# Performance work log

Measured on AMD Instinct MI355X. Metric: run time of the kernel, lower is better.

## Reference

```python
import jax, jax.numpy as jnp
import numpy as np
from functools import partial

E = 256   # input_size (embedding dim)
H = 256   # hidden_size
T = 4096  # number of admissions (GRU sequence length, batch=1)


def _gru_seq(x_seq, w_ih, w_hh, b_ih, b_hh):
    """Single-layer unidirectional GRU over x_seq [T, E] with batch=1.
    PyTorch gate order: r, z, n. Returns outputs [T, H]."""
    h_dim = w_hh.shape[1]
    # input projections are step-independent: precompute [T, 3H]
    gi_all = x_seq @ w_ih.T + b_ih

    def step(h, gi):
        gh = h @ w_hh.T + b_hh
        i_r, i_z, i_n = jnp.split(gi, 3)
        h_r, h_z, h_n = jnp.split(gh, 3)
        r = jax.nn.sigmoid(i_r + h_r)
        z = jax.nn.sigmoid(i_z + h_z)
        n = jnp.tanh(i_n + r * h_n)
        h_new = (1.0 - z) * n + z * h
        return h_new, h_new

    h0 = jnp.zeros((h_dim,), x_seq.dtype)
    _, out = jax.lax.scan(step, h0, gi_all)
    return out  # [T, H]


def setup_inputs() -> dict:
    key = jax.random.key(0)
    ks = jax.random.split(key, 16)
    u = lambda k, shape, s: jax.random.uniform(k, shape, jnp.float32, -s, s)
    sg = 1.0 / np.sqrt(H)  # PyTorch GRU/Linear init scale
    inp = {}
    # embeddings initialized uniform(-0.1, 0.1) per initialize_weights()
    inp["emb_diag"] = u(ks[0], (20000, E), 0.1)
    inp["emb_proc"] = u(ks[1], (15000, E), 0.1)  # unused by forward (source bug), kept for fidelity
    # GRU params (layer 0), gate order r,z,n
    inp["wih_d"] = u(ks[2], (3 * H, E), sg)
    inp["whh_d"] = u(ks[3], (3 * H, H), sg)
    inp["bih_d"] = u(ks[4], (3 * H,), sg)
    inp["bhh_d"] = u(ks[5], (3 * H,), sg)
    inp["wih_p"] = u(ks[6], (3 * H, E), sg)
    inp["whh_p"] = u(ks[7], (3 * H, H), sg)
    inp["bih_p"] = u(ks[8], (3 * H,), sg)
    inp["bhh_p"] = u(ks[9], (3 * H,), sg)
    # linear_embedding: ReLU -> Linear(2H, H)
    sl = 1.0 / np.sqrt(2 * H)
    inp["w_lin"] = u(ks[10], (H, 2 * H), sl)
    inp["b_lin"] = u(ks[11], (H,), sl)
    # ragged admission code lists, represented as fixed-length rows
    inp["diag_codes"] = jax.random.randint(ks[12], (T, 32), 0, 20000)
    inp["proc_codes"] = jax.random.randint(ks[13], (T, 16), 0, 15000)
    inp["input_medication"] = jax.random.randint(ks[14], (T, 24), 0, 3000)
    return inp


def reference(emb_diag, emb_proc, wih_d, whh_d, bih_d, bhh_d,
              wih_p, whh_p, bih_p, bhh_p, w_lin, b_lin,
              diag_codes, proc_codes, input_medication):
    # per-admission embedding gather + mean pool (dropout rate 0 -> identity)
    # NOTE: original source uses embedding_diagnoses for BOTH loops (bug kept).
    seq_d = emb_diag[diag_codes].mean(axis=1)  # [T, E]
    seq_p = emb_diag[proc_codes].mean(axis=1)  # [T, E]
    out_d = _gru_seq(seq_d, wih_d, whh_d, bih_d, bhh_d)  # [T, H]
    out_p = _gru_seq(seq_p, wih_p, whh_p, bih_p, bhh_p)  # [T, H]
    patient = jnp.concatenate([out_d, out_p], axis=-1)   # [T, 2H]
    queries = jax.nn.relu(patient) @ w_lin.T + b_lin     # [T, H]
    query = queries[-1:]
    memory_keys = queries[:-1]
    memory_values = input_medication[:-1]
    return (query, memory_keys, memory_values)
```

## Files before the change

kernel.cpp:

```cpp
#include <hip/hip_runtime.h>
#include <hip/hip_fp16.h>

#define T_SEQ 4096
#define E_DIM 256
#define H_DIM 256
#define G3    768

#define KEYS_OFF 256
#define MED_OFF  1048576

#define WS_SEQ_D   0
#define WS_SEQ_P   1048576
#define WS_GI_D    2097152
#define WS_GI_P    5242880
#define WS_PATIENT 8388608

#define SW_SCALE   2016.0f
#define SH_SCALE   127.0f
#define INV_SY     (1.0f / (2016.0f * 127.0f))

__device__ __forceinline__ float fast_rcp(float x) {
#if __has_builtin(__builtin_amdgcn_rcpf)
    return __builtin_amdgcn_rcpf(x);
#else
    return 1.f / x;
#endif
}

__device__ __forceinline__ int sdot4(int a, int b, int c) {
#if __has_builtin(__builtin_amdgcn_sdot4)
    return __builtin_amdgcn_sdot4(a, b, c, false);
#else
    c += ((a << 24) >> 24) * ((b << 24) >> 24);
    c += ((a << 16) >> 24) * ((b << 16) >> 24);
    c += ((a <<  8) >> 24) * ((b <<  8) >> 24);
    c += ( a        >> 24) * ( b        >> 24);
    return c;
#endif
}

__device__ __forceinline__ int pair_sum_i32(int x) {
#if __has_builtin(__builtin_amdgcn_update_dpp)
    x += __builtin_amdgcn_update_dpp(0, x, 0xB1 , 0xF, 0xF, true);
    return x;
#else
    x += __shfl_xor(x, 1);
    return x;
#endif
}

__global__ __launch_bounds__(256) void gather_mean_kernel(
    const float* __restrict__ emb, const int* __restrict__ dcodes,
    const int* __restrict__ pcodes, const int* __restrict__ med,
    float* __restrict__ seq_d, float* __restrict__ seq_p,
    float* __restrict__ med_out)
{
    const int t = blockIdx.x;
    const int e = threadIdx.x;
    __shared__ int cd[32];
    __shared__ int cp[16];
    if (e < 32) cd[e] = dcodes[t * 32 + e];
    else if (e < 48) cp[e - 32] = pcodes[t * 16 + (e - 32)];
    __syncthreads();

    float sd = 0.f;
#pragma unroll 4
    for (int i = 0; i < 32; i++) sd += emb[(size_t)cd[i] * E_DIM + e];
    seq_d[(size_t)t * E_DIM + e] = sd * (1.f / 32.f);

    float sp = 0.f;
#pragma unroll 4
    for (int i = 0; i < 16; i++) sp += emb[(size_t)cp[i] * E_DIM + e];
    seq_p[(size_t)t * E_DIM + e] = sp * (1.f / 16.f);

    if (t < T_SEQ - 1 && e < 24) med_out[t * 24 + e] = (float)med[t * 24 + e];
}

__global__ __launch_bounds__(256) void gemm_gi_kernel(
    const float* __restrict__ seq_d, const float* __restrict__ seq_p,
    const float* __restrict__ wih_d, const float* __restrict__ wih_p,
    const float* __restrict__ bih_d, const float* __restrict__ bih_p,
    const float* __restrict__ bhh_d, const float* __restrict__ bhh_p,
    float* __restrict__ gi_d, float* __restrict__ gi_p)
{
    const int K = E_DIM, N = G3;
    const float* A    = blockIdx.z ? seq_p : seq_d;
    const float* W    = blockIdx.z ? wih_p : wih_d;
    const float* bias = blockIdx.z ? bih_p : bih_d;
    const float* bhh  = blockIdx.z ? bhh_p : bhh_d;
    float*       C    = blockIdx.z ? gi_p  : gi_d;

    __shared__ float As[16][132];
    __shared__ float Bs[16][132];

    const int tid = threadIdx.x;
    const int tx = tid & 15, ty = tid >> 4;
    const int m0 = blockIdx.x * 128, n0 = blockIdx.y * 128;
    const int r = tid >> 2;
    const int c = (tid & 3) << 2;

    float acc[8][8];
#pragma unroll
    for (int i = 0; i < 8; i++)
#pragma unroll
        for (int j = 0; j < 8; j++) acc[i][j] = 0.f;

    for (int k0 = 0; k0 < K; k0 += 16) {
        float4 a0 = *(const float4*)&A[(size_t)(m0 + r) * K + k0 + c];
        float4 a1 = *(const float4*)&A[(size_t)(m0 + r + 64) * K + k0 + c];
        float4 b0 = *(const float4*)&W[(size_t)(n0 + r) * K + k0 + c];
        float4 b1 = *(const float4*)&W[(size_t)(n0 + r + 64) * K + k0 + c];
        As[c + 0][r] = a0.x; As[c + 1][r] = a0.y; As[c + 2][r] = a0.z; As[c + 3][r] = a0.w;
        As[c + 0][r + 64] = a1.x; As[c + 1][r + 64] = a1.y; As[c + 2][r + 64] = a1.z; As[c + 3][r + 64] = a1.w;
        Bs[c + 0][r] = b0.x; Bs[c + 1][r] = b0.y; Bs[c + 2][r] = b0.z; Bs[c + 3][r] = b0.w;
        Bs[c + 0][r + 64] = b1.x; Bs[c + 1][r + 64] = b1.y; Bs[c + 2][r + 64] = b1.z; Bs[c + 3][r + 64] = b1.w;
        __syncthreads();
#pragma unroll
        for (int k = 0; k < 16; k++) {
            float4 aa0 = *(const float4*)&As[k][ty * 8];
            float4 aa1 = *(const float4*)&As[k][ty * 8 + 4];
            float4 bb0 = *(const float4*)&Bs[k][tx * 8];
            float4 bb1 = *(const float4*)&Bs[k][tx * 8 + 4];
            float a[8] = {aa0.x, aa0.y, aa0.z, aa0.w, aa1.x, aa1.y, aa1.z, aa1.w};
            float b[8] = {bb0.x, bb0.y, bb0.z, bb0.w, bb1.x, bb1.y, bb1.z, bb1.w};
#pragma unroll
            for (int i = 0; i < 8; i++)
#pragma unroll
                for (int j = 0; j < 8; j++) acc[i][j] = fmaf(a[i], b[j], acc[i][j]);
        }
        __syncthreads();
    }

#pragma unroll
    for (int i = 0; i < 8; i++) {
        const int m = m0 + ty * 8 + i;
#pragma unroll
        for (int j = 0; j < 8; j++) {
            const int n = n0 + tx * 8 + j;
            const float bb = bias[n] + ((n < 512) ? bhh[n] : 0.f);
            C[(size_t)m * N + n] = acc[i][j] + bb;
        }
    }
}

__global__ __launch_bounds__(256) void quant_whh_kernel(
    const float* __restrict__ whh_d, const float* __restrict__ whh_p,
    unsigned int* __restrict__ w8_d, unsigned int* __restrict__ w8_p)
{
    const int idx = blockIdx.x * 256 + threadIdx.x;
    const float* src = blockIdx.y ? whh_p : whh_d;
    unsigned int* dst = blockIdx.y ? w8_p : w8_d;
    const float4 f = *(const float4*)&src[(size_t)idx * 4];
    const int b0 = (int)rintf(f.x * SW_SCALE) & 0xFF;
    const int b1 = (int)rintf(f.y * SW_SCALE) & 0xFF;
    const int b2 = (int)rintf(f.z * SW_SCALE) & 0xFF;
    const int b3 = (int)rintf(f.w * SW_SCALE) & 0xFF;
    dst[idx] = (unsigned int)(b0 | (b1 << 8) | (b2 << 16) | (b3 << 24));
}

__global__ __launch_bounds__(512, 2) void gru_scan_kernel(
    const unsigned int* __restrict__ w8_d, const unsigned int* __restrict__ w8_p,
    const float* __restrict__ bhh_d, const float* __restrict__ bhh_p,
    const float* __restrict__ gi_d, const float* __restrict__ gi_p,
    float* __restrict__ patient)
{
    const unsigned int* w8 = blockIdx.x ? w8_p : w8_d;
    const float* bhh = blockIdx.x ? bhh_p : bhh_d;
    const float* gi  = blockIdx.x ? gi_p  : gi_d;
    const int col_off = blockIdx.x ? H_DIM : 0;

    const int tid = threadIdx.x;
    const int l   = tid & 63;
    const int w   = tid >> 6;
    const int q   = 32 * w + (l >> 1);
    const int c   = l & 1;

    int wgt[3][32];
#pragma unroll
    for (int g = 0; g < 3; g++) {
        const int4* p = (const int4*)(w8 + ((size_t)(g * 256 + q) * 64 + c * 32));
#pragma unroll
        for (int i = 0; i < 8; i++) {
            const int4 v = p[i];
            wgt[g][4 * i + 0] = v.x;
            wgt[g][4 * i + 1] = v.y;
            wgt[g][4 * i + 2] = v.z;
            wgt[g][4 * i + 3] = v.w;
        }
    }

    __shared__ __align__(16) char hb[2][256];
    if (tid < 256) hb[0][tid] = 0;

    const bool gl = (c == 0);
    float h = 0.f, g0 = 0.f, g1 = 0.f, g2 = 0.f, b2f = 0.f;
    if (gl) {
        b2f = bhh[512 + q];
        g0 = gi[q]; g1 = gi[256 + q]; g2 = gi[512 + q];
    }
    const float* gi_t = gi + G3;
    float*       pat  = patient + col_off;

    const char* hrd = &hb[0][c * 128];

    __syncthreads();

#define GRU_STEP(PAR)                                                           \
    {                                                                           \
        float ng0 = 0.f, ng1 = 0.f, ng2 = 0.f;                                  \
        if (gl) { ng0 = gi_t[q]; ng1 = gi_t[256 + q]; ng2 = gi_t[512 + q]; }    \
        int a0 = 0, a1 = 0, a2 = 0;                                             \
        _Pragma("unroll")                                                       \
        for (int j = 0; j < 8; j++) {                                           \
            const uint4 H = *(const uint4*)(hrd + (PAR) * 256 + j * 16);        \
            const int x0 = (int)H.x, x1 = (int)H.y, x2 = (int)H.z, x3 = (int)H.w; \
            a0 = sdot4(wgt[0][4 * j + 0], x0, a0);                              \
            a0 = sdot4(wgt[0][4 * j + 1], x1, a0);                              \
            a0 = sdot4(wgt[0][4 * j + 2], x2, a0);                              \
            a0 = sdot4(wgt[0][4 * j + 3], x3, a0);                              \
            a1 = sdot4(wgt[1][4 * j + 0], x0, a1);                              \
            a1 = sdot4(wgt[1][4 * j + 1], x1, a1);                              \
            a1 = sdot4(wgt[1][4 * j + 2], x2, a1);                              \
            a1 = sdot4(wgt[1][4 * j + 3], x3, a1);                              \
            a2 = sdot4(wgt[2][4 * j + 0], x0, a2);                              \
            a2 = sdot4(wgt[2][4 * j + 1], x1, a2);                              \
            a2 = sdot4(wgt[2][4 * j + 2], x2, a2);                              \
            a2 = sdot4(wgt[2][4 * j + 3], x3, a2);                              \
        }                                                                       \
        a0 = pair_sum_i32(a0);                                                  \
        a1 = pair_sum_i32(a1);                                                  \
        a2 = pair_sum_i32(a2);                                                  \
        if (gl) {                                                               \
            const float y0 = (float)a0 * INV_SY;                                \
            const float y1 = (float)a1 * INV_SY;                                \
            const float y2 = (float)a2 * INV_SY;                                \
            const float xr = g0 + y0;                 \
            const float xz = g1 + y1;                 \
            const float rr = fast_rcp(1.f + __expf(-xr));                       \
            const float zz = fast_rcp(1.f + __expf(-xz));                       \
            float xn = g2 + rr * (y2 + b2f);                                    \
            xn = fminf(fmaxf(xn, -15.f), 15.f);                                 \
            const float e2 = __expf(2.f * xn);                                  \
            const float nn = (e2 - 1.f) * fast_rcp(e2 + 1.f);                   \
            h = nn + zz * (h - nn);                                             \
            hb[(PAR) ^ 1][q] = (char)(int)rintf(h * SH_SCALE);                  \
            pat[q] = h;                                                         \
            g0 = ng0; g1 = ng1; g2 = ng2;                                       \
        }                                                                       \
        gi_t += G3;                                                             \
        pat += 512;                                                             \
        __syncthreads();                                                        \
    }

    for (int t = 0; t < T_SEQ; t += 2) {
        GRU_STEP(0)
        GRU_STEP(1)
    }
#undef GRU_STEP
}

__global__ __launch_bounds__(256) void gemm_fin_kernel(
    const float* __restrict__ patient, const float* __restrict__ w_lin,
    const float* __restrict__ b_lin, float* __restrict__ out)
{
    const int K = 512, N = H_DIM;

    __shared__ float As[16][132];
    __shared__ float Bs[16][132];

    const int tid = threadIdx.x;
    const int tx = tid & 15, ty = tid >> 4;
    const int m0 = blockIdx.x * 128, n0 = blockIdx.y * 128;
    const int r = tid >> 2;
    const int c = (tid & 3) << 2;

    float acc[8][8];
#pragma unroll
    for (int i = 0; i < 8; i++)
#pragma unroll
        for (int j = 0; j < 8; j++) acc[i][j] = 0.f;

    for (int k0 = 0; k0 < K; k0 += 16) {
        float4 a0 = *(const float4*)&patient[(size_t)(m0 + r) * K + k0 + c];
        float4 a1 = *(const float4*)&patient[(size_t)(m0 + r + 64) * K + k0 + c];
        float4 b0 = *(const float4*)&w_lin[(size_t)(n0 + r) * K + k0 + c];
        float4 b1 = *(const float4*)&w_lin[(size_t)(n0 + r + 64) * K + k0 + c];
        a0.x = fmaxf(a0.x, 0.f); a0.y = fmaxf(a0.y, 0.f); a0.z = fmaxf(a0.z, 0.f); a0.w = fmaxf(a0.w, 0.f);
        a1.x = fmaxf(a1.x, 0.f); a1.y = fmaxf(a1.y, 0.f); a1.z = fmaxf(a1.z, 0.f); a1.w = fmaxf(a1.w, 0.f);
        As[c + 0][r] = a0.x; As[c + 1][r] = a0.y; As[c + 2][r] = a0.z; As[c + 3][r] = a0.w;
        As[c + 0][r + 64] = a1.x; As[c + 1][r + 64] = a1.y; As[c + 2][r + 64] = a1.z; As[c + 3][r + 64] = a1.w;
        Bs[c + 0][r] = b0.x; Bs[c + 1][r] = b0.y; Bs[c + 2][r] = b0.z; Bs[c + 3][r] = b0.w;
        Bs[c + 0][r + 64] = b1.x; Bs[c + 1][r + 64] = b1.y; Bs[c + 2][r + 64] = b1.z; Bs[c + 3][r + 64] = b1.w;
        __syncthreads();
#pragma unroll
        for (int k = 0; k < 16; k++) {
            float4 aa0 = *(const float4*)&As[k][ty * 8];
            float4 aa1 = *(const float4*)&As[k][ty * 8 + 4];
            float4 bb0 = *(const float4*)&Bs[k][tx * 8];
            float4 bb1 = *(const float4*)&Bs[k][tx * 8 + 4];
            float a[8] = {aa0.x, aa0.y, aa0.z, aa0.w, aa1.x, aa1.y, aa1.z, aa1.w};
            float b[8] = {bb0.x, bb0.y, bb0.z, bb0.w, bb1.x, bb1.y, bb1.z, bb1.w};
#pragma unroll
            for (int i = 0; i < 8; i++)
#pragma unroll
                for (int j = 0; j < 8; j++) acc[i][j] = fmaf(a[i], b[j], acc[i][j]);
        }
        __syncthreads();
    }

#pragma unroll
    for (int i = 0; i < 8; i++) {
        const int m = m0 + ty * 8 + i;
#pragma unroll
        for (int j = 0; j < 8; j++) {
            const int n = n0 + tx * 8 + j;
            const float v = acc[i][j] + b_lin[n];
            if (m == T_SEQ - 1) out[n] = v;
            else out[KEYS_OFF + (size_t)m * H_DIM + n] = v;
        }
    }
}

extern "C" void kernel_launch(void* const* d_in, const int* in_sizes, int n_in,
                              void* d_out, int out_size, void* d_ws, size_t ws_size,
                              hipStream_t stream)
{
    const float* emb_diag = (const float*)d_in[0];
    const float* wih_d = (const float*)d_in[2];
    const float* whh_d = (const float*)d_in[3];
    const float* bih_d = (const float*)d_in[4];
    const float* bhh_d = (const float*)d_in[5];
    const float* wih_p = (const float*)d_in[6];
    const float* whh_p = (const float*)d_in[7];
    const float* bih_p = (const float*)d_in[8];
    const float* bhh_p = (const float*)d_in[9];
    const float* w_lin = (const float*)d_in[10];
    const float* b_lin = (const float*)d_in[11];
    const int* dcodes = (const int*)d_in[12];
    const int* pcodes = (const int*)d_in[13];
    const int* med    = (const int*)d_in[14];

    float* out = (float*)d_out;
    float* ws  = (float*)d_ws;

    float* seq_d   = ws + WS_SEQ_D;
    float* seq_p   = ws + WS_SEQ_P;
    float* gi_d    = ws + WS_GI_D;
    float* gi_p    = ws + WS_GI_P;
    float* patient = ws + WS_PATIENT;
    unsigned int* w8_d = (unsigned int*)(ws + WS_SEQ_D);
    unsigned int* w8_p = (unsigned int*)(ws + WS_SEQ_P);

    gather_mean_kernel<<<T_SEQ, 256, 0, stream>>>(
        emb_diag, dcodes, pcodes, med, seq_d, seq_p, out + MED_OFF);

    gemm_gi_kernel<<<dim3(32, 6, 2), 256, 0, stream>>>(
        seq_d, seq_p, wih_d, wih_p, bih_d, bih_p, bhh_d, bhh_p, gi_d, gi_p);

    quant_whh_kernel<<<dim3(192, 2), 256, 0, stream>>>(
        whh_d, whh_p, w8_d, w8_p);

    gru_scan_kernel<<<2, 512, 0, stream>>>(
        w8_d, w8_p, bhh_d, bhh_p, gi_d, gi_p, patient);

    gemm_fin_kernel<<<dim3(32, 2, 1), 256, 0, stream>>>(
        patient, w_lin, b_lin, out);
}
```

Baseline: 2.969 ms.

## Give each GRU thread a full hidden row and broadcast h via readlane

The sequential GRU scan now runs with 256 threads per block, one per hidden unit, holding all 64 packed int8 weight words per gate in registers (192 registers of weights). The old pairwise split with its DPP reduction is removed. The hidden state is read as one int per lane from LDS and broadcast with readlane, and each quad packs its four int8 h values with DPP ORs so only one thread writes them to shared memory. This aims to cut the LDS traffic and the cross-lane reduction in each step, and to synchronise fewer waves per step. The cost is very high register pressure (possible spills) and 64 serial readlane operations in every step.

```diff
diff --git a/kernel.cpp b/kernel.cpp
--- a/kernel.cpp
+++ b/kernel.cpp
@@ -39,13 +39,23 @@
 #endif
 }
 
-__device__ __forceinline__ int pair_sum_i32(int x) {
+__device__ __forceinline__ int quad_or_i32(int x) {
 #if __has_builtin(__builtin_amdgcn_update_dpp)
-    x += __builtin_amdgcn_update_dpp(0, x, 0xB1 , 0xF, 0xF, true);
+    x |= __builtin_amdgcn_update_dpp(0, x, 0xB1 , 0xF, 0xF, true);
+    x |= __builtin_amdgcn_update_dpp(0, x, 0x4E , 0xF, 0xF, true);
     return x;
 #else
-    x += __shfl_xor(x, 1);
+    x |= __shfl_xor(x, 1);
+    x |= __shfl_xor(x, 2);
     return x;
+#endif
+}
+
+__device__ __forceinline__ int rdlane(int v, int l) {
+#if __has_builtin(__builtin_amdgcn_readlane)
+    return __builtin_amdgcn_readlane(v, l);
+#else
+    return __shfl(v, l);
 #endif
 }
 
@@ -158,7 +168,7 @@
     dst[idx] = (unsigned int)(b0 | (b1 << 8) | (b2 << 16) | (b3 << 24));
 }
 
-__global__ __launch_bounds__(512, 2) void gru_scan_kernel(
+__global__ __launch_bounds__(256, 1) void gru_scan_kernel(
     const unsigned int* __restrict__ w8_d, const unsigned int* __restrict__ w8_p,
     const float* __restrict__ bhh_d, const float* __restrict__ bhh_p,
     const float* __restrict__ gi_d, const float* __restrict__ gi_p,
@@ -169,18 +179,15 @@
     const float* gi  = blockIdx.x ? gi_p  : gi_d;
     const int col_off = blockIdx.x ? H_DIM : 0;
 
-    const int tid = threadIdx.x;
-    const int l   = tid & 63;
-    const int w   = tid >> 6;
-    const int q   = 32 * w + (l >> 1);
-    const int c   = l & 1;
-
-    int wgt[3][32];
+    const int q    = threadIdx.x;
+    const int lane = q & 63;
+
+    int wgt[3][64];
 #pragma unroll
     for (int g = 0; g < 3; g++) {
-        const int4* p = (const int4*)(w8 + ((size_t)(g * 256 + q) * 64 + c * 32));
-#pragma unroll
-        for (int i = 0; i < 8; i++) {
+        const int4* p = (const int4*)(w8 + (size_t)(g * 256 + q) * 64);
+#pragma unroll
+        for (int i = 0; i < 16; i++) {
             const int4 v = p[i];
             wgt[g][4 * i + 0] = v.x;
             wgt[g][4 * i + 1] = v.y;
@@ -190,63 +197,48 @@
     }
 
     __shared__ __align__(16) char hb[2][256];
-    if (tid < 256) hb[0][tid] = 0;
-
-    const bool gl = (c == 0);
-    float h = 0.f, g0 = 0.f, g1 = 0.f, g2 = 0.f, b2f = 0.f;
-    if (gl) {
-        b2f = bhh[512 + q];
-        g0 = gi[q]; g1 = gi[256 + q]; g2 = gi[512 + q];
-    }
+    hb[0][q] = 0;
+
+    float h = 0.f;
+    const float b2f = bhh[512 + q];
+    float g0 = gi[q], g1 = gi[256 + q], g2 = gi[512 + q];
     const float* gi_t = gi + G3;
     float*       pat  = patient + col_off;
-
-    const char* hrd = &hb[0][c * 128];
+    const int shl = (q & 3) * 8;
 
     __syncthreads();
 
 #define GRU_STEP(PAR)                                                           \
     {                                                                           \
-        float ng0 = 0.f, ng1 = 0.f, ng2 = 0.f;                                  \
-        if (gl) { ng0 = gi_t[q]; ng1 = gi_t[256 + q]; ng2 = gi_t[512 + q]; }    \
+        const float ng0 = gi_t[q];                                              \
+        const float ng1 = gi_t[256 + q];                                        \
+        const float ng2 = gi_t[512 + q];                                        \
+        const int hvec = *(const int*)&hb[PAR][lane * 4];                       \
         int a0 = 0, a1 = 0, a2 = 0;                                             \
         _Pragma("unroll")                                                       \
-        for (int j = 0; j < 8; j++) {                                           \
-            const uint4 H = *(const uint4*)(hrd + (PAR) * 256 + j * 16);        \
-            const int x0 = (int)H.x, x1 = (int)H.y, x2 = (int)H.z, x3 = (int)H.w; \
-            a0 = sdot4(wgt[0][4 * j + 0], x0, a0);                              \
-            a0 = sdot4(wgt[0][4 * j + 1], x1, a0);                              \
-            a0 = sdot4(wgt[0][4 * j + 2], x2, a0);                              \
-            a0 = sdot4(wgt[0][4 * j + 3], x3, a0);                              \
-            a1 = sdot4(wgt[1][4 * j + 0], x0, a1);                              \
-            a1 = sdot4(wgt[1][4 * j + 1], x1, a1);                              \
-            a1 = sdot4(wgt[1][4 * j + 2], x2, a1);                              \
-            a1 = sdot4(wgt[1][4 * j + 3], x3, a1);                              \
-            a2 = sdot4(wgt[2][4 * j + 0], x0, a2);                              \
-            a2 = sdot4(wgt[2][4 * j + 1], x1, a2);                              \
-            a2 = sdot4(wgt[2][4 * j + 2], x2, a2);                              \
-            a2 = sdot4(wgt[2][4 * j + 3], x3, a2);                              \
+        for (int j = 0; j < 64; j++) {                                          \
+            const int hj = rdlane(hvec, j);                                     \
+            a0 = sdot4(wgt[0][j], hj, a0);                                      \
+            a1 = sdot4(wgt[1][j], hj, a1);                                      \
+            a2 = sdot4(wgt[2][j], hj, a2);                                      \
         }                                                                       \
-        a0 = pair_sum_i32(a0);                                                  \
-        a1 = pair_sum_i32(a1);                                                  \
-        a2 = pair_sum_i32(a2);                                                  \
-        if (gl) {                                                               \
-            const float y0 = (float)a0 * INV_SY;                                \
-            const float y1 = (float)a1 * INV_SY;                                \
-            const float y2 = (float)a2 * INV_SY;                                \
-            const float xr = g0 + y0;                 \
-            const float xz = g1 + y1;                 \
-            const float rr = fast_rcp(1.f + __expf(-xr));                       \
-            const float zz = fast_rcp(1.f + __expf(-xz));                       \
-            float xn = g2 + rr * (y2 + b2f);                                    \
-            xn = fminf(fmaxf(xn, -15.f), 15.f);                                 \
-            const float e2 = __expf(2.f * xn);                                  \
-            const float nn = (e2 - 1.f) * fast_rcp(e2 + 1.f);                   \
-            h = nn + zz * (h - nn);                                             \
-            hb[(PAR) ^ 1][q] = (char)(int)rintf(h * SH_SCALE);                  \
-            pat[q] = h;                                                         \
-            g0 = ng0; g1 = ng1; g2 = ng2;                                       \
-        }                                                                       \
+        const float y0 = (float)a0 * INV_SY;                                    \
+        const float y1 = (float)a1 * INV_SY;                                    \
+        const float y2 = (float)a2 * INV_SY;                                    \
+        const float xr = g0 + y0;                     \
+        const float xz = g1 + y1;                     \
+        const float rr = fast_rcp(1.f + __expf(-xr));                           \
+        const float zz = fast_rcp(1.f + __expf(-xz));                           \
+        float xn = g2 + rr * (y2 + b2f);                                        \
+        xn = fminf(fmaxf(xn, -15.f), 15.f);                                     \
+        const float e2 = __expf(2.f * xn);                                      \
+        const float nn = (e2 - 1.f) * fast_rcp(e2 + 1.f);                       \
+        h = nn + zz * (h - nn);                                                 \
+        int b = (((int)rintf(h * SH_SCALE)) & 0xFF) << shl;                     \
+        b = quad_or_i32(b);                                                     \
+        if ((q & 3) == 0) *(int*)&hb[(PAR) ^ 1][q] = b;                         \
+        pat[q] = h;                                                             \
+        g0 = ng0; g1 = ng1; g2 = ng2;                                           \
         gi_t += G3;                                                             \
         pat += 512;                                                             \
         __syncthreads();                                                        \
@@ -360,7 +352,7 @@
     quant_whh_kernel<<<dim3(192, 2), 256, 0, stream>>>(
         whh_d, whh_p, w8_d, w8_p);
 
-    gru_scan_kernel<<<2, 512, 0, stream>>>(
+    gru_scan_kernel<<<2, 256, 0, stream>>>(
         w8_d, w8_p, bhh_d, bhh_p, gi_d, gi_p, patient);
 
     gemm_fin_kernel<<<dim3(32, 2, 1), 256, 0, stream>>>(
```

Measured after the change: 3.517 ms. 18.5% more time.
